# Kernel tuning notes

Hardware: AMD Instinct MI355X
Metric: run time of the kernel (lower is better)

The kernel has to match this reference:

```python
import jax, jax.numpy as jnp
import numpy as np

B, L, D, DF, E, R = 4, 1024, 1024, 4096, 32768, 64
EPS = 1e-6


def layer_norm(x, g, b, eps=EPS):
    mu = x.mean(-1, keepdims=True)
    var = ((x - mu) ** 2).mean(-1, keepdims=True)
    return (x - mu) * jax.lax.rsqrt(var + eps) * g + b


def setup_inputs() -> dict:
    key = jax.random.key(0)
    ks = jax.random.split(key, 16)
    s = 0.02
    return {
        "hidden_states": jax.random.normal(ks[0], (B, L, D), jnp.float32),
        "rel_table": jax.random.normal(ks[1], (R, D), jnp.float32) * s,
        "Wq": jax.random.normal(ks[2], (D, D), jnp.float32) * s,
        "bq": jnp.zeros((D,), jnp.float32),
        "Wk": jax.random.normal(ks[3], (D, D), jnp.float32) * s,
        "Wv": jax.random.normal(ks[4], (D, D), jnp.float32) * s,
        "Wo": jax.random.normal(ks[5], (D, D), jnp.float32) * s,
        "bo": jnp.zeros((D,), jnp.float32),
        "ln0_g": jnp.ones((D,), jnp.float32),
        "ln0_b": jnp.zeros((D,), jnp.float32),
        "ln1_g": jnp.ones((D,), jnp.float32),
        "ln1_b": jnp.zeros((D,), jnp.float32),
        "W1": jax.random.normal(ks[6], (D, DF), jnp.float32) * s,
        "b1": jnp.zeros((DF,), jnp.float32),
        "W2": jax.random.normal(ks[7], (DF, D), jnp.float32) * s,
        "b2": jnp.zeros((D,), jnp.float32),
        "ln2_g": jnp.ones((D,), jnp.float32),
        "ln2_b": jnp.zeros((D,), jnp.float32),
        "edge_src": jax.random.randint(ks[8], (B, E), 0, L, jnp.int32),
        "edge_dst": jax.random.randint(ks[9], (B, E), 0, L, jnp.int32),
        "edge_rel": jax.random.randint(ks[10], (B, E), 0, R, jnp.int32),
    }


def reference(hidden_states, rel_table, Wq, bq, Wk, Wv, Wo, bo,
              ln0_g, ln0_b, ln1_g, ln1_b, W1, b1, W2, b2, ln2_g, ln2_b,
              edge_src, edge_dst, edge_rel):
    scale = np.sqrt(D).astype(np.float32)  # num_heads=1 -> d_k = D
    hs_norm = layer_norm(hidden_states, ln0_g, ln0_b)

    def rgat_one(x, src, dst, rel):
        # x: [L, D]; src/dst/rel: [E]
        e = rel_table[rel]                       # [E, D] relation embeddings
        q = x @ Wq + bq
        k = x @ Wk
        v = x @ Wv
        score = jnp.sum((k[src] + e) * q[dst], axis=-1) / scale      # [E]
        score = jnp.exp(jnp.clip(score, -10.0, 10.0))
        wv = jax.ops.segment_sum((v[src] + e) * score[:, None], dst, num_segments=L)
        z = jax.ops.segment_sum(score, dst, num_segments=L)          # [L]
        o = wv / z[:, None]
        out = layer_norm(x + o @ Wo + bo, ln1_g, ln1_b)
        ffn = jnp.maximum(out @ W1 + b1, 0.0) @ W2 + b2
        return layer_norm(out + ffn, ln2_g, ln2_b)

    graph_rep = jax.vmap(rgat_one)(hs_norm, edge_src, edge_dst, edge_rel)
    out = jax.nn.elu(graph_rep)                  # dropout = identity (eval)
    return hidden_states + out
```

## Files before the change

kernel.cpp:

```cpp
#include <hip/hip_runtime.h>
#include <hip/hip_bf16.h>

#define B_SZ 4
#define L_SEQ 1024
#define D_MODEL 1024
#define DF_FF 4096
#define E_PER_B 32768
#define R_REL 64
#define M_ROWS (B_SZ * L_SEQ)

typedef __attribute__((ext_vector_type(8))) short bf16x8;
typedef __attribute__((ext_vector_type(4))) float f32x4;

__device__ inline float b2f(unsigned short u) {
    union { unsigned int i; float f; } x; x.i = ((unsigned int)u) << 16; return x.f;
}
__device__ inline unsigned short f2b(float f) {
    union { float f; unsigned int u; } x; x.f = f;
    unsigned int r = x.u + 0x7FFFu + ((x.u >> 16) & 1u);
    return (unsigned short)(r >> 16);
}

#define GLOBAL_CAST(p) ((const __attribute__((address_space(1))) void*)(p))
#define LDS_CAST(p)    ((__attribute__((address_space(3))) void*)(p))

__global__ void transpose_f32_to_bf16(const float* __restrict__ W,
                                      unsigned short* __restrict__ Wt,
                                      int K, int N) {
    __shared__ float tile[32][33];
    int n0 = blockIdx.x * 32, k0 = blockIdx.y * 32;
    int tx = threadIdx.x & 31, ty = threadIdx.x >> 5;
#pragma unroll
    for (int r = 0; r < 32; r += 8)
        tile[ty + r][tx] = W[(size_t)(k0 + ty + r) * N + (n0 + tx)];
    __syncthreads();
#pragma unroll
    for (int r = 0; r < 32; r += 8)
        Wt[(size_t)(n0 + ty + r) * K + (k0 + tx)] = f2b(tile[tx][ty + r]);
}

__global__ void transpose_v_bf16(const unsigned short* __restrict__ QKV,
                                 unsigned short* __restrict__ Vt) {
    __shared__ unsigned short tile[32][33];
    const int b = blockIdx.z;
    const int d0 = blockIdx.x * 32, s0 = blockIdx.y * 32;
    const int tx = threadIdx.x & 31, ty = threadIdx.x >> 5;
#pragma unroll
    for (int r = 0; r < 32; r += 8)
        tile[ty + r][tx] = QKV[(size_t)((b << 10) + s0 + ty + r) * 3072 + 2048 + d0 + tx];
    __syncthreads();
#pragma unroll
    for (int r = 0; r < 32; r += 8)
        Vt[(size_t)b * 1048576 + (size_t)(d0 + ty + r) * 1024 + s0 + tx] = tile[tx][ty + r];
}

__global__ void build_bqkv(const float* __restrict__ bq, float* __restrict__ bqkv) {
    int i = blockIdx.x * 256 + threadIdx.x;
    bqkv[i] = (i < 1024) ? bq[i] : 0.0f;
}

__global__ void build_relbpad(const float* __restrict__ rel, unsigned short* __restrict__ out) {
    int i = blockIdx.x * 256 + threadIdx.x;
    out[i] = (i < 65536) ? f2b(rel[i]) : (unsigned short)0;
}

__global__ void build_relbT(const float* __restrict__ rel, unsigned short* __restrict__ out) {
    int i = blockIdx.x * 256 + threadIdx.x;
    int d = i >> 6, r = i & 63;
    out[i] = f2b(rel[r * 1024 + d]);
}

__device__ inline void tile_swizzle(int id, int ntn, int& tm, int& tn) {
    tm = ((id & 7) + ((id >> 3) / ntn) * 8) * 128;
    tn = ((id >> 3) % ntn) * 128;
}

template<bool OUT_BF16, bool RELU, bool ACC>
__global__ __launch_bounds__(256, 4)
void gemm_bf16(const unsigned short* __restrict__ A, int lda,
               const unsigned short* __restrict__ Bt, int ldb, size_t bt_batch,
               const float* __restrict__ bias,
               float* __restrict__ Cf, unsigned short* __restrict__ Cb,
               const float* __restrict__ accin,
               int N, int K, int ntn) {
    __shared__ unsigned short lA[128 * 64];
    __shared__ unsigned short lB[128 * 64];
    int tile_m, tile_n;
    tile_swizzle(blockIdx.x, ntn, tile_m, tile_n);
    const int t = threadIdx.x;
    const int wave = t >> 6, lane = t & 63;
    const int wm = (wave >> 1) * 64, wn = (wave & 1) * 64;
    const int quad = lane >> 4, l16 = lane & 15;

    const int srow = lane >> 3;
    const int schunk = ((lane & 7) ^ srow) * 8;
    const unsigned short* gA = A + (size_t)(tile_m + wave * 32 + srow) * lda + schunk;
    const unsigned short* gB = Bt + (size_t)(tile_m >> 10) * bt_batch
                                  + (size_t)(tile_n + wave * 32 + srow) * ldb + schunk;

    f32x4 acc[4][4];
#pragma unroll
    for (int i = 0; i < 4; i++)
#pragma unroll
        for (int j = 0; j < 4; j++) acc[i][j] = (f32x4)0.0f;

    for (int k0 = 0; k0 < K; k0 += 64) {
        __syncthreads();
#pragma unroll
        for (int r = 0; r < 4; ++r) {
            __builtin_amdgcn_global_load_lds(GLOBAL_CAST(gA + (size_t)r * 8 * lda),
                                             LDS_CAST(&lA[(wave * 32 + r * 8) * 64]), 16, 0, 0);
            __builtin_amdgcn_global_load_lds(GLOBAL_CAST(gB + (size_t)r * 8 * ldb),
                                             LDS_CAST(&lB[(wave * 32 + r * 8) * 64]), 16, 0, 0);
        }
        gA += 64; gB += 64;
        __builtin_amdgcn_s_waitcnt(0);
        __syncthreads();

#pragma unroll
        for (int kk = 0; kk < 2; ++kk) {
            const int cb = kk * 4 + quad;
            bf16x8 af[4], bf[4];
#pragma unroll
            for (int i = 0; i < 4; i++) {
                const int ra = wm + i * 16 + l16;
                af[i] = *(const bf16x8*)&lA[ra * 64 + ((cb ^ (ra & 7)) * 8)];
                const int rb = wn + i * 16 + l16;
                bf[i] = *(const bf16x8*)&lB[rb * 64 + ((cb ^ (rb & 7)) * 8)];
            }
#pragma unroll
            for (int mi = 0; mi < 4; mi++)
#pragma unroll
                for (int ni = 0; ni < 4; ni++)
                    acc[mi][ni] = __builtin_amdgcn_mfma_f32_16x16x32_bf16(af[mi], bf[ni], acc[mi][ni], 0, 0, 0);
        }
    }

#pragma unroll
    for (int mi = 0; mi < 4; mi++) {
#pragma unroll
        for (int ni = 0; ni < 4; ni++) {
            const int col = tile_n + wn + ni * 16 + l16;
            const float bv = bias[col];
#pragma unroll
            for (int r = 0; r < 4; r++) {
                const int row = tile_m + wm + mi * 16 + quad * 4 + r;
                float v = acc[mi][ni][r] + bv;
                if (ACC) v += accin[(size_t)row * N + col];
                if (RELU) v = fmaxf(v, 0.0f);
                if (OUT_BF16) Cb[(size_t)row * N + col] = f2b(v);
                else          Cf[(size_t)row * N + col] = v;
            }
        }
    }
}

__global__ __launch_bounds__(256, 4)
void gemm_bf16_splitk(const unsigned short* __restrict__ A, int lda,
                      const unsigned short* __restrict__ Bt, int ldb, size_t bt_batch,
                      const float* __restrict__ bias,
                      float* __restrict__ Pbase, size_t pstride,
                      int N, int Kc, int ntn) {
    __shared__ unsigned short lA[128 * 64];
    __shared__ unsigned short lB[128 * 64];
    int tile_m, tile_n;
    tile_swizzle(blockIdx.x, ntn, tile_m, tile_n);
    const int z = blockIdx.z;
    const int kofs = z * Kc;
    const int t = threadIdx.x;
    const int wave = t >> 6, lane = t & 63;
    const int wm = (wave >> 1) * 64, wn = (wave & 1) * 64;
    const int quad = lane >> 4, l16 = lane & 15;

    const int srow = lane >> 3;
    const int schunk = ((lane & 7) ^ srow) * 8;
    const unsigned short* gA = A + (size_t)(tile_m + wave * 32 + srow) * lda + kofs + schunk;
    const unsigned short* gB = Bt + (size_t)(tile_m >> 10) * bt_batch
                                  + (size_t)(tile_n + wave * 32 + srow) * ldb + kofs + schunk;

    f32x4 acc[4][4];
#pragma unroll
    for (int i = 0; i < 4; i++)
#pragma unroll
        for (int j = 0; j < 4; j++) acc[i][j] = (f32x4)0.0f;

    for (int k0 = 0; k0 < Kc; k0 += 64) {
        __syncthreads();
#pragma unroll
        for (int r = 0; r < 4; ++r) {
            __builtin_amdgcn_global_load_lds(GLOBAL_CAST(gA + (size_t)r * 8 * lda),
                                             LDS_CAST(&lA[(wave * 32 + r * 8) * 64]), 16, 0, 0);
            __builtin_amdgcn_global_load_lds(GLOBAL_CAST(gB + (size_t)r * 8 * ldb),
                                             LDS_CAST(&lB[(wave * 32 + r * 8) * 64]), 16, 0, 0);
        }
        gA += 64; gB += 64;
        __builtin_amdgcn_s_waitcnt(0);
        __syncthreads();

#pragma unroll
        for (int kk = 0; kk < 2; ++kk) {
            const int cb = kk * 4 + quad;
            bf16x8 af[4], bf[4];
#pragma unroll
            for (int i = 0; i < 4; i++) {
                const int ra = wm + i * 16 + l16;
                af[i] = *(const bf16x8*)&lA[ra * 64 + ((cb ^ (ra & 7)) * 8)];
                const int rb = wn + i * 16 + l16;
                bf[i] = *(const bf16x8*)&lB[rb * 64 + ((cb ^ (rb & 7)) * 8)];
            }
#pragma unroll
            for (int mi = 0; mi < 4; mi++)
#pragma unroll
                for (int ni = 0; ni < 4; ni++)
                    acc[mi][ni] = __builtin_amdgcn_mfma_f32_16x16x32_bf16(af[mi], bf[ni], acc[mi][ni], 0, 0, 0);
        }
    }

    float* P = Pbase + (size_t)z * pstride;
#pragma unroll
    for (int mi = 0; mi < 4; mi++) {
#pragma unroll
        for (int ni = 0; ni < 4; ni++) {
            const int col = tile_n + wn + ni * 16 + l16;
            const float bv = (z == 0) ? bias[col] : 0.0f;
#pragma unroll
            for (int r = 0; r < 4; r++) {
                const int row = tile_m + wm + mi * 16 + quad * 4 + r;
                P[(size_t)row * N + col] = acc[mi][ni][r] + bv;
            }
        }
    }
}

template<int MODE, int NR>
__global__ void ln_kernel(const float* __restrict__ X, const unsigned short* __restrict__ Xb,
                          const float* __restrict__ Rbase, size_t rstride,
                          const float* __restrict__ g, const float* __restrict__ be,
                          float* __restrict__ of32, unsigned short* __restrict__ ob16,
                          const float* __restrict__ hidden, float* __restrict__ fout) {
    __shared__ float sb1[4], sb2[4];
    const int row = blockIdx.x, t = threadIdx.x;
    const size_t base = (size_t)row * 1024 + t * 4;

    float x0, x1, x2, x3;
    if (MODE == 2) {
        ushort4 xv = *(const ushort4*)(Xb + base);
        x0 = b2f(xv.x); x1 = b2f(xv.y); x2 = b2f(xv.z); x3 = b2f(xv.w);
    } else {
        float4 xv = *(const float4*)(X + base);
        x0 = xv.x; x1 = xv.y; x2 = xv.z; x3 = xv.w;
    }
#pragma unroll
    for (int r = 0; r < NR; r++) {
        float4 rv = *(const float4*)(Rbase + r * rstride + base);
        x0 += rv.x; x1 += rv.y; x2 += rv.z; x3 += rv.w;
    }
    float s = x0 + x1 + x2 + x3;
#pragma unroll
    for (int o = 32; o > 0; o >>= 1) s += __shfl_down(s, o);
    if ((t & 63) == 0) sb1[t >> 6] = s;
    __syncthreads();
    const float mu = (sb1[0] + sb1[1] + sb1[2] + sb1[3]) * (1.0f / 1024.0f);

    const float d0 = x0 - mu, d1 = x1 - mu, d2 = x2 - mu, d3 = x3 - mu;
    float s2 = d0 * d0 + d1 * d1 + d2 * d2 + d3 * d3;
#pragma unroll
    for (int o = 32; o > 0; o >>= 1) s2 += __shfl_down(s2, o);
    if ((t & 63) == 0) sb2[t >> 6] = s2;
    __syncthreads();
    const float var = (sb2[0] + sb2[1] + sb2[2] + sb2[3]) * (1.0f / 1024.0f);
    const float rstd = rsqrtf(var + 1e-6f);

    const float4 gv = *(const float4*)(g + t * 4);
    const float4 bv = *(const float4*)(be + t * 4);
    const float y0 = d0 * rstd * gv.x + bv.x;
    const float y1 = d1 * rstd * gv.y + bv.y;
    const float y2 = d2 * rstd * gv.z + bv.z;
    const float y3 = d3 * rstd * gv.w + bv.w;

    if (MODE == 0) {
        float4 o; o.x = y0; o.y = y1; o.z = y2; o.w = y3;
        *(float4*)(of32 + base) = o;
    }
    if (MODE <= 1) {
        ushort4 ob; ob.x = f2b(y0); ob.y = f2b(y1); ob.z = f2b(y2); ob.w = f2b(y3);
        *(ushort4*)(ob16 + base) = ob;
    } else {
        const float4 hv = *(const float4*)(hidden + base);
        const float e0 = y0 > 0.0f ? y0 : expm1f(y0);
        const float e1 = y1 > 0.0f ? y1 : expm1f(y1);
        const float e2 = y2 > 0.0f ? y2 : expm1f(y2);
        const float e3 = y3 > 0.0f ? y3 : expm1f(y3);
        float4 o; o.x = hv.x + e0; o.y = hv.y + e1; o.z = hv.z + e2; o.w = hv.w + e3;
        *(float4*)(fout + base) = o;
    }
}

__global__ void edge_scatter(const float* __restrict__ S0, const float* __restrict__ S1,
                             const float* __restrict__ T,
                             const int* __restrict__ src, const int* __restrict__ dst,
                             const int* __restrict__ rel,
                             float* __restrict__ A, float* __restrict__ G) {
    const int gg = blockIdx.x * 256 + threadIdx.x;
    const int b = gg >> 15;
    const int s = src[gg], d = dst[gg], r = rel[gg];
    const size_t srow = (size_t)((b << 10) + s) * 1024 + d;
    const float sval = S0[srow] + S1[srow];
    const float tval = T[(size_t)((b << 10) + d) * 128 + r];
    float sc = (sval + tval) * (1.0f / 32.0f);
    sc = expf(fminf(fmaxf(sc, -10.0f), 10.0f));
    atomicAdd(&A[((size_t)((b << 10) + d) << 10) + s], sc);
    atomicAdd(&G[((size_t)((b << 10) + d) << 6) + r], sc);
}

__global__ void zrow_convG(const float* __restrict__ G, float* __restrict__ rz,
                           unsigned short* __restrict__ Gn) {
    const int node = blockIdx.x * 4 + (threadIdx.x >> 6);
    const int lane = threadIdx.x & 63;
    const float v = G[(size_t)node * 64 + lane];
    float s = v;
#pragma unroll
    for (int o = 1; o < 64; o <<= 1) s += __shfl_xor(s, o);
    const float inv = 1.0f / s;
    Gn[(size_t)node * 64 + lane] = f2b(v * inv);
    if (lane == 0) rz[node] = inv;
}

__global__ void convA(const float* __restrict__ A, const float* __restrict__ rz,
                      unsigned short* __restrict__ An) {
    const int row = blockIdx.x, t = threadIdx.x;
    const float r = rz[row];
    const size_t base = (size_t)row * 1024 + t * 4;
    const float4 v = *(const float4*)(A + base);
    ushort4 o;
    o.x = f2b(v.x * r); o.y = f2b(v.y * r); o.z = f2b(v.z * r); o.w = f2b(v.w * r);
    *(ushort4*)(An + base) = o;
}

extern "C" void kernel_launch(void* const* d_in, const int* in_sizes, int n_in,
                              void* d_out, int out_size, void* d_ws, size_t ws_size,
                              hipStream_t stream) {
    const float* hidden  = (const float*)d_in[0];
    const float* rel_tbl = (const float*)d_in[1];
    const float* Wq = (const float*)d_in[2];
    const float* bq = (const float*)d_in[3];
    const float* Wk = (const float*)d_in[4];
    const float* Wv = (const float*)d_in[5];
    const float* Wo = (const float*)d_in[6];
    const float* bo = (const float*)d_in[7];
    const float* ln0_g = (const float*)d_in[8];
    const float* ln0_b = (const float*)d_in[9];
    const float* ln1_g = (const float*)d_in[10];
    const float* ln1_b = (const float*)d_in[11];
    const float* W1 = (const float*)d_in[12];
    const float* b1 = (const float*)d_in[13];
    const float* W2 = (const float*)d_in[14];
    const float* b2 = (const float*)d_in[15];
    const float* ln2_g = (const float*)d_in[16];
    const float* ln2_b = (const float*)d_in[17];
    const int* esrc = (const int*)d_in[18];
    const int* edst = (const int*)d_in[19];
    const int* erel = (const int*)d_in[20];
    float* out = (float*)d_out;

    char* ws = (char*)d_ws;
    const size_t MB = 1024 * 1024;
    float*          Xn_f32  = (float*)(ws + 0);
    unsigned short* Xn_b16  = (unsigned short*)(ws + 16 * MB);
    unsigned short* Vt      = (unsigned short*)(ws + 16 * MB);
    unsigned short* H1      = (unsigned short*)(ws + 0);
    unsigned short* Wqkv_t  = (unsigned short*)(ws + 24 * MB);
    unsigned short* Wo_t    = (unsigned short*)(ws + 30 * MB);
    unsigned short* Out_b16 = (unsigned short*)(ws + 113 * MB);
    unsigned short* W1_t    = (unsigned short*)(ws + 32 * MB);
    unsigned short* W2_t    = (unsigned short*)(ws + 40 * MB);
    unsigned short* relbPad = (unsigned short*)(ws + 48 * MB);
    unsigned short* relbT   = (unsigned short*)(ws + 48 * MB + 256 * 1024);
    float*          bqkv    = (float*)(ws + 48 * MB + 512 * 1024);
    const float*    zbias   = bqkv + 1024;
    unsigned short* QKV     = (unsigned short*)(ws + 49 * MB);
    float*          Amat    = (float*)(ws + 49 * MB);
    float*          Gmat    = (float*)(ws + 65 * MB);
    float*          rz      = (float*)(ws + 66 * MB);
    float*          Pwo     = (float*)(ws + 49 * MB);
    float*          Qw2     = (float*)(ws + 49 * MB);
    float*          S0      = (float*)(ws + 73 * MB);
    float*          tmp     = (float*)(ws + 73 * MB);
    unsigned short* Obf     = (unsigned short*)(ws + 89 * MB);
    unsigned short* An      = (unsigned short*)(ws + 97 * MB);
    float*          Tmat    = (float*)(ws + 105 * MB);
    unsigned short* Gn      = (unsigned short*)(ws + 105 * MB);

    const size_t PSTRIDE = 4u * 1024 * 1024;
    const size_t BT_QKV  = 1024u * 3072;
    const size_t BT_VT   = 1024u * 1024;
    const dim3 blk(256);

    transpose_f32_to_bf16<<<dim3(32, 32), blk, 0, stream>>>(Wq, Wqkv_t, 1024, 1024);
    transpose_f32_to_bf16<<<dim3(32, 32), blk, 0, stream>>>(Wk, Wqkv_t + 1024 * 1024, 1024, 1024);
    transpose_f32_to_bf16<<<dim3(32, 32), blk, 0, stream>>>(Wv, Wqkv_t + 2 * 1024 * 1024, 1024, 1024);
    transpose_f32_to_bf16<<<dim3(32, 32), blk, 0, stream>>>(Wo, Wo_t, 1024, 1024);
    transpose_f32_to_bf16<<<dim3(128, 32), blk, 0, stream>>>(W1, W1_t, 1024, 4096);
    transpose_f32_to_bf16<<<dim3(32, 128), blk, 0, stream>>>(W2, W2_t, 4096, 1024);
    build_relbpad<<<512, blk, 0, stream>>>(rel_tbl, relbPad);
    build_relbT<<<256, blk, 0, stream>>>(rel_tbl, relbT);
    build_bqkv<<<12, blk, 0, stream>>>(bq, bqkv);

    ln_kernel<0, 0><<<M_ROWS, blk, 0, stream>>>(hidden, nullptr, nullptr, 0, ln0_g, ln0_b,
                                                Xn_f32, Xn_b16, nullptr, nullptr);
    gemm_bf16<true, false, false><<<dim3(24 * 32), blk, 0, stream>>>(
        Xn_b16, 1024, Wqkv_t, 1024, 0, bqkv, nullptr, QKV, nullptr, 3072, 1024, 24);
    transpose_v_bf16<<<dim3(32, 32, 4), blk, 0, stream>>>(QKV, Vt);
    gemm_bf16_splitk<<<dim3(8 * 32, 1, 2), blk, 0, stream>>>(
        QKV + 1024, 3072, QKV, 3072, BT_QKV, zbias, S0, PSTRIDE, 1024, 512, 8);
    gemm_bf16<false, false, false><<<dim3(1 * 32), blk, 0, stream>>>(
        QKV, 3072, relbPad, 1024, 0, zbias, Tmat, nullptr, nullptr, 128, 1024, 1);
    hipMemsetAsync(ws + 49 * MB, 0, 17 * MB + 16 * 1024, stream);
    edge_scatter<<<512, blk, 0, stream>>>(S0, S0 + PSTRIDE, Tmat, esrc, edst, erel, Amat, Gmat);
    zrow_convG<<<1024, blk, 0, stream>>>(Gmat, rz, Gn);
    convA<<<M_ROWS, blk, 0, stream>>>(Amat, rz, An);
    gemm_bf16<false, false, false><<<dim3(8 * 32), blk, 0, stream>>>(
        Gn, 64, relbT, 64, 0, zbias, tmp, nullptr, nullptr, 1024, 64, 8);
    gemm_bf16<true, false, true><<<dim3(8 * 32), blk, 0, stream>>>(
        An, 1024, Vt, 1024, BT_VT, zbias, nullptr, Obf, tmp, 1024, 1024, 8);
    gemm_bf16_splitk<<<dim3(8 * 32, 1, 2), blk, 0, stream>>>(
        Obf, 1024, Wo_t, 1024, 0, bo, Pwo, PSTRIDE, 1024, 512, 8);
    ln_kernel<1, 2><<<M_ROWS, blk, 0, stream>>>(Xn_f32, nullptr, Pwo, PSTRIDE, ln1_g, ln1_b,
                                                nullptr, Out_b16, nullptr, nullptr);
    gemm_bf16<true, true, false><<<dim3(32 * 32), blk, 0, stream>>>(
        Out_b16, 1024, W1_t, 1024, 0, b1, nullptr, H1, nullptr, 4096, 1024, 32);
    gemm_bf16_splitk<<<dim3(8 * 32, 1, 4), blk, 0, stream>>>(
        H1, 4096, W2_t, 4096, 0, b2, Qw2, PSTRIDE, 1024, 1024, 8);
    ln_kernel<2, 4><<<M_ROWS, blk, 0, stream>>>(nullptr, Out_b16, Qw2, PSTRIDE, ln2_g, ln2_b,
                                                nullptr, nullptr, hidden, out);
    (void)in_sizes; (void)n_in; (void)out_size; (void)ws_size;
}
```

Before: 427.3 us.

## Store split-K partials in bf16, merge prep kernels, fuse normalization kernels

The split-K GEMM partial outputs (attention scores, Wo and W2 partials) are now written and read as bf16 instead of fp32, which halves the traffic for those intermediates in the GEMM epilogue, edge_scatter and the layernorm kernels. The nine weight-prep launches are merged into one prep_all kernel. The zrow_convG and convA kernels are fused into a single normalize kernel that no longer writes the rz buffer. In exchange, the partial sums are rounded to bf16 before they are reduced, which loses precision and could push outputs past tolerance.

```diff
diff --git a/kernel.cpp b/kernel.cpp
--- a/kernel.cpp
+++ b/kernel.cpp
@@ -24,19 +24,48 @@
 #define GLOBAL_CAST(p) ((const __attribute__((address_space(1))) void*)(p))
 #define LDS_CAST(p)    ((__attribute__((address_space(3))) void*)(p))
 
-__global__ void transpose_f32_to_bf16(const float* __restrict__ W,
-                                      unsigned short* __restrict__ Wt,
-                                      int K, int N) {
+__global__ void prep_all(const float* __restrict__ Wq, const float* __restrict__ Wk,
+                         const float* __restrict__ Wv, const float* __restrict__ Wo,
+                         const float* __restrict__ W1, const float* __restrict__ W2,
+                         const float* __restrict__ rel, const float* __restrict__ bq,
+                         unsigned short* __restrict__ Wqkv_t, unsigned short* __restrict__ Wo_t,
+                         unsigned short* __restrict__ W1_t, unsigned short* __restrict__ W2_t,
+                         unsigned short* __restrict__ relbPad, unsigned short* __restrict__ relbT,
+                         float* __restrict__ bqkv) {
     __shared__ float tile[32][33];
-    int n0 = blockIdx.x * 32, k0 = blockIdx.y * 32;
-    int tx = threadIdx.x & 31, ty = threadIdx.x >> 5;
-#pragma unroll
-    for (int r = 0; r < 32; r += 8)
-        tile[ty + r][tx] = W[(size_t)(k0 + ty + r) * N + (n0 + tx)];
-    __syncthreads();
-#pragma unroll
-    for (int r = 0; r < 32; r += 8)
-        Wt[(size_t)(n0 + ty + r) * K + (k0 + tx)] = f2b(tile[tx][ty + r]);
+    const int id = blockIdx.x, tid = threadIdx.x;
+    if (id < 12288) {
+        const float* src; unsigned short* dst; int K, N, x, y;
+        if (id < 4096) {
+            const int seg = id >> 10, t = id & 1023;
+            K = 1024; N = 1024; x = t & 31; y = t >> 5;
+            src = (seg == 0) ? Wq : (seg == 1) ? Wk : (seg == 2) ? Wv : Wo;
+            dst = (seg == 3) ? Wo_t : (Wqkv_t + (size_t)seg * 1048576);
+        } else if (id < 8192) {
+            const int t = id - 4096; K = 1024; N = 4096; x = t & 127; y = t >> 7;
+            src = W1; dst = W1_t;
+        } else {
+            const int t = id - 8192; K = 4096; N = 1024; x = t & 31; y = t >> 5;
+            src = W2; dst = W2_t;
+        }
+        const int n0 = x * 32, k0 = y * 32, tx = tid & 31, ty = tid >> 5;
+#pragma unroll
+        for (int r = 0; r < 32; r += 8)
+            tile[ty + r][tx] = src[(size_t)(k0 + ty + r) * N + (n0 + tx)];
+        __syncthreads();
+#pragma unroll
+        for (int r = 0; r < 32; r += 8)
+            dst[(size_t)(n0 + ty + r) * K + (k0 + tx)] = f2b(tile[tx][ty + r]);
+    } else if (id < 12800) {
+        const int i = (id - 12288) * 256 + tid;
+        relbPad[i] = (i < 65536) ? f2b(rel[i]) : (unsigned short)0;
+    } else if (id < 13056) {
+        const int i = (id - 12800) * 256 + tid;
+        relbT[i] = f2b(rel[(i & 63) * 1024 + (i >> 6)]);
+    } else {
+        const int i = (id - 13056) * 256 + tid;
+        bqkv[i] = (i < 1024) ? bq[i] : 0.0f;
+    }
 }
 
 __global__ void transpose_v_bf16(const unsigned short* __restrict__ QKV,
@@ -52,22 +81,6 @@
 #pragma unroll
     for (int r = 0; r < 32; r += 8)
         Vt[(size_t)b * 1048576 + (size_t)(d0 + ty + r) * 1024 + s0 + tx] = tile[tx][ty + r];
-}
-
-__global__ void build_bqkv(const float* __restrict__ bq, float* __restrict__ bqkv) {
-    int i = blockIdx.x * 256 + threadIdx.x;
-    bqkv[i] = (i < 1024) ? bq[i] : 0.0f;
-}
-
-__global__ void build_relbpad(const float* __restrict__ rel, unsigned short* __restrict__ out) {
-    int i = blockIdx.x * 256 + threadIdx.x;
-    out[i] = (i < 65536) ? f2b(rel[i]) : (unsigned short)0;
-}
-
-__global__ void build_relbT(const float* __restrict__ rel, unsigned short* __restrict__ out) {
-    int i = blockIdx.x * 256 + threadIdx.x;
-    int d = i >> 6, r = i & 63;
-    out[i] = f2b(rel[r * 1024 + d]);
 }
 
 __device__ inline void tile_swizzle(int id, int ntn, int& tm, int& tn) {
@@ -159,7 +172,7 @@
 void gemm_bf16_splitk(const unsigned short* __restrict__ A, int lda,
                       const unsigned short* __restrict__ Bt, int ldb, size_t bt_batch,
                       const float* __restrict__ bias,
-                      float* __restrict__ Pbase, size_t pstride,
+                      unsigned short* __restrict__ Pbase, size_t pstride,
                       int N, int Kc, int ntn) {
     __shared__ unsigned short lA[128 * 64];
     __shared__ unsigned short lB[128 * 64];
@@ -216,7 +229,7 @@
         }
     }
 
-    float* P = Pbase + (size_t)z * pstride;
+    unsigned short* P = Pbase + (size_t)z * pstride;
 #pragma unroll
     for (int mi = 0; mi < 4; mi++) {
 #pragma unroll
@@ -226,7 +239,7 @@
 #pragma unroll
             for (int r = 0; r < 4; r++) {
                 const int row = tile_m + wm + mi * 16 + quad * 4 + r;
-                P[(size_t)row * N + col] = acc[mi][ni][r] + bv;
+                P[(size_t)row * N + col] = f2b(acc[mi][ni][r] + bv);
             }
         }
     }
@@ -234,7 +247,7 @@
 
 template<int MODE, int NR>
 __global__ void ln_kernel(const float* __restrict__ X, const unsigned short* __restrict__ Xb,
-                          const float* __restrict__ Rbase, size_t rstride,
+                          const unsigned short* __restrict__ Rbase, size_t rstride,
                           const float* __restrict__ g, const float* __restrict__ be,
                           float* __restrict__ of32, unsigned short* __restrict__ ob16,
                           const float* __restrict__ hidden, float* __restrict__ fout) {
@@ -252,8 +265,8 @@
     }
 #pragma unroll
     for (int r = 0; r < NR; r++) {
-        float4 rv = *(const float4*)(Rbase + r * rstride + base);
-        x0 += rv.x; x1 += rv.y; x2 += rv.z; x3 += rv.w;
+        ushort4 rv = *(const ushort4*)(Rbase + r * rstride + base);
+        x0 += b2f(rv.x); x1 += b2f(rv.y); x2 += b2f(rv.z); x3 += b2f(rv.w);
     }
     float s = x0 + x1 + x2 + x3;
 #pragma unroll
@@ -296,7 +309,8 @@
     }
 }
 
-__global__ void edge_scatter(const float* __restrict__ S0, const float* __restrict__ S1,
+__global__ void edge_scatter(const unsigned short* __restrict__ S0h,
+                             const unsigned short* __restrict__ S1h,
                              const float* __restrict__ T,
                              const int* __restrict__ src, const int* __restrict__ dst,
                              const int* __restrict__ rel,
@@ -305,7 +319,7 @@
     const int b = gg >> 15;
     const int s = src[gg], d = dst[gg], r = rel[gg];
     const size_t srow = (size_t)((b << 10) + s) * 1024 + d;
-    const float sval = S0[srow] + S1[srow];
+    const float sval = b2f(S0h[srow]) + b2f(S1h[srow]);
     const float tval = T[(size_t)((b << 10) + d) * 128 + r];
     float sc = (sval + tval) * (1.0f / 32.0f);
     sc = expf(fminf(fmaxf(sc, -10.0f), 10.0f));
@@ -313,27 +327,25 @@
     atomicAdd(&G[((size_t)((b << 10) + d) << 6) + r], sc);
 }
 
-__global__ void zrow_convG(const float* __restrict__ G, float* __restrict__ rz,
-                           unsigned short* __restrict__ Gn) {
-    const int node = blockIdx.x * 4 + (threadIdx.x >> 6);
-    const int lane = threadIdx.x & 63;
-    const float v = G[(size_t)node * 64 + lane];
-    float s = v;
-#pragma unroll
-    for (int o = 1; o < 64; o <<= 1) s += __shfl_xor(s, o);
-    const float inv = 1.0f / s;
-    Gn[(size_t)node * 64 + lane] = f2b(v * inv);
-    if (lane == 0) rz[node] = inv;
-}
-
-__global__ void convA(const float* __restrict__ A, const float* __restrict__ rz,
-                      unsigned short* __restrict__ An) {
+__global__ void normalize(const float* __restrict__ A, const float* __restrict__ G,
+                          unsigned short* __restrict__ An, unsigned short* __restrict__ Gn) {
+    __shared__ float sInv;
     const int row = blockIdx.x, t = threadIdx.x;
-    const float r = rz[row];
+    float v = 0.0f;
+    if (t < 64) {
+        v = G[(size_t)row * 64 + t];
+        float s = v;
+#pragma unroll
+        for (int o = 1; o < 64; o <<= 1) s += __shfl_xor(s, o);
+        if (t == 0) sInv = 1.0f / s;
+    }
+    __syncthreads();
+    const float inv = sInv;
+    if (t < 64) Gn[(size_t)row * 64 + t] = f2b(v * inv);
     const size_t base = (size_t)row * 1024 + t * 4;
-    const float4 v = *(const float4*)(A + base);
+    const float4 a = *(const float4*)(A + base);
     ushort4 o;
-    o.x = f2b(v.x * r); o.y = f2b(v.y * r); o.z = f2b(v.z * r); o.w = f2b(v.w * r);
+    o.x = f2b(a.x * inv); o.y = f2b(a.y * inv); o.z = f2b(a.z * inv); o.w = f2b(a.w * inv);
     *(ushort4*)(An + base) = o;
 }
 
@@ -371,7 +383,6 @@
     unsigned short* H1      = (unsigned short*)(ws + 0);
     unsigned short* Wqkv_t  = (unsigned short*)(ws + 24 * MB);
     unsigned short* Wo_t    = (unsigned short*)(ws + 30 * MB);
-    unsigned short* Out_b16 = (unsigned short*)(ws + 113 * MB);
     unsigned short* W1_t    = (unsigned short*)(ws + 32 * MB);
     unsigned short* W2_t    = (unsigned short*)(ws + 40 * MB);
     unsigned short* relbPad = (unsigned short*)(ws + 48 * MB);
@@ -381,57 +392,48 @@
     unsigned short* QKV     = (unsigned short*)(ws + 49 * MB);
     float*          Amat    = (float*)(ws + 49 * MB);
     float*          Gmat    = (float*)(ws + 65 * MB);
-    float*          rz      = (float*)(ws + 66 * MB);
-    float*          Pwo     = (float*)(ws + 49 * MB);
-    float*          Qw2     = (float*)(ws + 49 * MB);
-    float*          S0      = (float*)(ws + 73 * MB);
+    unsigned short* PwoH    = (unsigned short*)(ws + 49 * MB);
+    unsigned short* Qw2H    = (unsigned short*)(ws + 49 * MB);
+    unsigned short* S0h     = (unsigned short*)(ws + 73 * MB);
     float*          tmp     = (float*)(ws + 73 * MB);
     unsigned short* Obf     = (unsigned short*)(ws + 89 * MB);
     unsigned short* An      = (unsigned short*)(ws + 97 * MB);
     float*          Tmat    = (float*)(ws + 105 * MB);
     unsigned short* Gn      = (unsigned short*)(ws + 105 * MB);
-
-    const size_t PSTRIDE = 4u * 1024 * 1024;
+    unsigned short* Out_b16 = (unsigned short*)(ws + 113 * MB);
+
+    const size_t PSTRIDE_H = 4u * 1024 * 1024;
     const size_t BT_QKV  = 1024u * 3072;
     const size_t BT_VT   = 1024u * 1024;
     const dim3 blk(256);
 
-    transpose_f32_to_bf16<<<dim3(32, 32), blk, 0, stream>>>(Wq, Wqkv_t, 1024, 1024);
-    transpose_f32_to_bf16<<<dim3(32, 32), blk, 0, stream>>>(Wk, Wqkv_t + 1024 * 1024, 1024, 1024);
-    transpose_f32_to_bf16<<<dim3(32, 32), blk, 0, stream>>>(Wv, Wqkv_t + 2 * 1024 * 1024, 1024, 1024);
-    transpose_f32_to_bf16<<<dim3(32, 32), blk, 0, stream>>>(Wo, Wo_t, 1024, 1024);
-    transpose_f32_to_bf16<<<dim3(128, 32), blk, 0, stream>>>(W1, W1_t, 1024, 4096);
-    transpose_f32_to_bf16<<<dim3(32, 128), blk, 0, stream>>>(W2, W2_t, 4096, 1024);
-    build_relbpad<<<512, blk, 0, stream>>>(rel_tbl, relbPad);
-    build_relbT<<<256, blk, 0, stream>>>(rel_tbl, relbT);
-    build_bqkv<<<12, blk, 0, stream>>>(bq, bqkv);
-
+    prep_all<<<13068, blk, 0, stream>>>(Wq, Wk, Wv, Wo, W1, W2, rel_tbl, bq,
+                                        Wqkv_t, Wo_t, W1_t, W2_t, relbPad, relbT, bqkv);
     ln_kernel<0, 0><<<M_ROWS, blk, 0, stream>>>(hidden, nullptr, nullptr, 0, ln0_g, ln0_b,
                                                 Xn_f32, Xn_b16, nullptr, nullptr);
     gemm_bf16<true, false, false><<<dim3(24 * 32), blk, 0, stream>>>(
         Xn_b16, 1024, Wqkv_t, 1024, 0, bqkv, nullptr, QKV, nullptr, 3072, 1024, 24);
     transpose_v_bf16<<<dim3(32, 32, 4), blk, 0, stream>>>(QKV, Vt);
     gemm_bf16_splitk<<<dim3(8 * 32, 1, 2), blk, 0, stream>>>(
-        QKV + 1024, 3072, QKV, 3072, BT_QKV, zbias, S0, PSTRIDE, 1024, 512, 8);
+        QKV + 1024, 3072, QKV, 3072, BT_QKV, zbias, S0h, PSTRIDE_H, 1024, 512, 8);
     gemm_bf16<false, false, false><<<dim3(1 * 32), blk, 0, stream>>>(
         QKV, 3072, relbPad, 1024, 0, zbias, Tmat, nullptr, nullptr, 128, 1024, 1);
-    hipMemsetAsync(ws + 49 * MB, 0, 17 * MB + 16 * 1024, stream);
-    edge_scatter<<<512, blk, 0, stream>>>(S0, S0 + PSTRIDE, Tmat, esrc, edst, erel, Amat, Gmat);
-    zrow_convG<<<1024, blk, 0, stream>>>(Gmat, rz, Gn);
-    convA<<<M_ROWS, blk, 0, stream>>>(Amat, rz, An);
+    hipMemsetAsync(ws + 49 * MB, 0, 17 * MB, stream);
+    edge_scatter<<<512, blk, 0, stream>>>(S0h, S0h + PSTRIDE_H, Tmat, esrc, edst, erel, Amat, Gmat);
+    normalize<<<M_ROWS, blk, 0, stream>>>(Amat, Gmat, An, Gn);
     gemm_bf16<false, false, false><<<dim3(8 * 32), blk, 0, stream>>>(
         Gn, 64, relbT, 64, 0, zbias, tmp, nullptr, nullptr, 1024, 64, 8);
     gemm_bf16<true, false, true><<<dim3(8 * 32), blk, 0, stream>>>(
         An, 1024, Vt, 1024, BT_VT, zbias, nullptr, Obf, tmp, 1024, 1024, 8);
     gemm_bf16_splitk<<<dim3(8 * 32, 1, 2), blk, 0, stream>>>(
-        Obf, 1024, Wo_t, 1024, 0, bo, Pwo, PSTRIDE, 1024, 512, 8);
-    ln_kernel<1, 2><<<M_ROWS, blk, 0, stream>>>(Xn_f32, nullptr, Pwo, PSTRIDE, ln1_g, ln1_b,
+        Obf, 1024, Wo_t, 1024, 0, bo, PwoH, PSTRIDE_H, 1024, 512, 8);
+    ln_kernel<1, 2><<<M_ROWS, blk, 0, stream>>>(Xn_f32, nullptr, PwoH, PSTRIDE_H, ln1_g, ln1_b,
                                                 nullptr, Out_b16, nullptr, nullptr);
     gemm_bf16<true, true, false><<<dim3(32 * 32), blk, 0, stream>>>(
         Out_b16, 1024, W1_t, 1024, 0, b1, nullptr, H1, nullptr, 4096, 1024, 32);
     gemm_bf16_splitk<<<dim3(8 * 32, 1, 4), blk, 0, stream>>>(
-        H1, 4096, W2_t, 4096, 0, b2, Qw2, PSTRIDE, 1024, 1024, 8);
-    ln_kernel<2, 4><<<M_ROWS, blk, 0, stream>>>(nullptr, Out_b16, Qw2, PSTRIDE, ln2_g, ln2_b,
+        H1, 4096, W2_t, 4096, 0, b2, Qw2H, PSTRIDE_H, 1024, 1024, 8);
+    ln_kernel<2, 4><<<M_ROWS, blk, 0, stream>>>(nullptr, Out_b16, Qw2H, PSTRIDE_H, ln2_g, ln2_b,
                                                 nullptr, nullptr, hidden, out);
     (void)in_sizes; (void)n_in; (void)out_size; (void)ws_size;
 }
```

Result: faster. 402.0 us (-5.9%).
